# Kernel tuning notes

Hardware: AMD Instinct MI355X
Metric: run time of the kernel (lower is better)

Reference implementation:

```python
import jax, jax.numpy as jnp
import numpy as np
from jax import lax

B, T, PRED, F, L, H = 128, 512, 24, 16, 8, 1024


def _gru_cell(x, h, Wih, Whh, bih, bhh):
    # PyTorch GRU gate math. gi/gh: [B, 3H] in (r, z, n) order.
    gi = x @ Wih.T + bih
    gh = h @ Whh.T + bhh
    i_r, i_z, i_n = jnp.split(gi, 3, axis=-1)
    h_r, h_z, h_n = jnp.split(gh, 3, axis=-1)
    r = jax.nn.sigmoid(i_r + h_r)
    z = jax.nn.sigmoid(i_z + h_z)
    n = jnp.tanh(i_n + r * h_n)
    return (1.0 - z) * n + z * h


def _run_layer(x_seq, Wih, Whh, bih, bhh):
    # x_seq: [B, T, D] -> (outputs [B, T, H], h_T [B, H]); zero initial state as in torch default.
    h0 = jnp.zeros((x_seq.shape[0], Whh.shape[1]), x_seq.dtype)

    def step(h, x_t):
        h = _gru_cell(x_t, h, Wih, Whh, bih, bhh)
        return h, h

    hT, hs = lax.scan(step, h0, jnp.swapaxes(x_seq, 0, 1))
    return jnp.swapaxes(hs, 0, 1), hT


def setup_inputs() -> dict:
    key = jax.random.key(0)
    ks = jax.random.split(key, 20)
    s_in = 1.0 / np.sqrt(H)  # torch default uniform bound ~ 1/sqrt(H); use scaled normal
    d = {
        'feats': jax.random.normal(ks[0], (B, T + PRED - 1, F), jnp.float32),
        'labels': jax.random.normal(ks[1], (B, T, L), jnp.float32),
        'y': jax.random.normal(ks[2], (B, PRED - 1, L), jnp.float32),
        'teacher': 0,
        'enc_Wih0': jax.random.normal(ks[3], (3 * H, F + L), jnp.float32) * s_in,
        'enc_Whh0': jax.random.normal(ks[4], (3 * H, H), jnp.float32) * s_in,
        'enc_bih0': jax.random.normal(ks[5], (3 * H,), jnp.float32) * s_in,
        'enc_bhh0': jax.random.normal(ks[6], (3 * H,), jnp.float32) * s_in,
        'enc_Wih1': jax.random.normal(ks[7], (3 * H, H), jnp.float32) * s_in,
        'enc_Whh1': jax.random.normal(ks[8], (3 * H, H), jnp.float32) * s_in,
        'enc_bih1': jax.random.normal(ks[9], (3 * H,), jnp.float32) * s_in,
        'enc_bhh1': jax.random.normal(ks[10], (3 * H,), jnp.float32) * s_in,
        'dec_Wih': jax.random.normal(ks[11], (3 * H, F + L), jnp.float32) * s_in,
        'dec_Whh': jax.random.normal(ks[12], (3 * H, H), jnp.float32) * s_in,
        'dec_bih': jax.random.normal(ks[13], (3 * H,), jnp.float32) * s_in,
        'dec_bhh': jax.random.normal(ks[14], (3 * H,), jnp.float32) * s_in,
        'fc_W': jax.random.normal(ks[15], (L, H), jnp.float32) * s_in,
        'fc_b': jax.random.normal(ks[16], (L,), jnp.float32) * s_in,
    }
    return d


def reference(feats, labels, y, teacher,
              enc_Wih0, enc_Whh0, enc_bih0, enc_bhh0,
              enc_Wih1, enc_Whh1, enc_bih1, enc_bhh1,
              dec_Wih, dec_Whh, dec_bih, dec_bhh,
              fc_W, fc_b):
    seq_len = labels.shape[1]
    prior = feats[:, :seq_len]                 # [B, T, F]
    post = feats[:, seq_len:]                  # [B, PRED-1, F]
    x = jnp.concatenate([prior, labels], -1)   # [B, T, F+L]

    # 2-layer batch_first GRU encoder; take last layer's output at final time step.
    out0, _ = _run_layer(x, enc_Wih0, enc_Whh0, enc_bih0, enc_bhh0)
    _, h = _run_layer(out0, enc_Wih1, enc_Whh1, enc_bih1, enc_bhh1)  # h: [B, H]

    ps = h @ fc_W.T + fc_b                     # [B, L]
    post_t = jnp.swapaxes(post, 0, 1)          # [PRED-1, B, F]

    if teacher:
        y_t = jnp.swapaxes(y, 0, 1)            # [PRED-1, B, L]

        def step(h, xs):
            f_t, y_i = xs
            xin = jnp.concatenate([f_t, y_i], -1)
            h = _gru_cell(xin, h, dec_Wih, dec_Whh, dec_bih, dec_bhh)
            return h, h @ fc_W.T + fc_b

        _, outs = lax.scan(step, h, (post_t, y_t))
    else:
        def step(carry, f_t):
            h, p = carry
            xin = jnp.concatenate([f_t, p], -1)
            h = _gru_cell(xin, h, dec_Wih, dec_Whh, dec_bih, dec_bhh)
            p = h @ fc_W.T + fc_b
            return (h, p), p

        _, outs = lax.scan(step, (h, ps), post_t)

    return jnp.concatenate([ps[None], outs], 0)  # [PRED, B, L]
```

## Files before the change

### kernel.cpp

```cpp
#include <hip/hip_runtime.h>
#include <cstdint>
#include <cstddef>


typedef _Float16 f16;
typedef f16 f16x8 __attribute__((ext_vector_type(8)));
typedef float f32x4 __attribute__((ext_vector_type(4)));

#define NB 208
#define NT 512
#define H_ 1024
#define HSLOT 131072
#define GSLOT 393216

__device__ __forceinline__ float sigm(float x) { return 1.0f / (1.0f + __expf(-x)); }

__device__ __forceinline__ void gbar(int* flags, int* rel, int phase) {
  __syncthreads();
  const int tid = threadIdx.x;
  if (blockIdx.x == 0) {
    if (tid == 0) {
      __builtin_amdgcn_fence(__ATOMIC_RELEASE, "agent");
      __hip_atomic_store(&flags[0], phase, __ATOMIC_RELAXED, __HIP_MEMORY_SCOPE_AGENT);
    }
    if (tid < NB) {
      while (__hip_atomic_load(&flags[tid], __ATOMIC_RELAXED, __HIP_MEMORY_SCOPE_AGENT) < phase)
        __builtin_amdgcn_s_sleep(1);
    }
    __syncthreads();
    if (tid == 0) {
      __hip_atomic_store(rel, phase, __ATOMIC_RELAXED, __HIP_MEMORY_SCOPE_AGENT);
      __builtin_amdgcn_fence(__ATOMIC_ACQUIRE, "agent");
    }
  } else {
    if (tid == 0) {
      __builtin_amdgcn_fence(__ATOMIC_RELEASE, "agent");
      __hip_atomic_store(&flags[blockIdx.x], phase, __ATOMIC_RELAXED, __HIP_MEMORY_SCOPE_AGENT);
      while (__hip_atomic_load(rel, __ATOMIC_RELAXED, __HIP_MEMORY_SCOPE_AGENT) < phase)
        __builtin_amdgcn_s_sleep(1);
      __builtin_amdgcn_fence(__ATOMIC_ACQUIRE, "agent");
    }
  }
  __syncthreads();
}

__device__ __forceinline__ void fastbar(int* flags2, int* done, int fph, int nl,
                                        bool lead) {
  __syncthreads();
  const int tid = threadIdx.x;
  if (tid == 0)
    __hip_atomic_store(&flags2[blockIdx.x], fph, __ATOMIC_RELAXED, __HIP_MEMORY_SCOPE_AGENT);
  if (lead) {
    if (tid < NB) {
      while (__hip_atomic_load(&flags2[tid], __ATOMIC_RELAXED, __HIP_MEMORY_SCOPE_AGENT) < fph)
        __builtin_amdgcn_s_sleep(1);
    }
    __syncthreads();
    if (tid == 0) {
      __builtin_amdgcn_fence(__ATOMIC_RELEASE, "agent");
      if ((fph & 3) == 0)
        __builtin_amdgcn_fence(__ATOMIC_ACQUIRE, "agent");
      __hip_atomic_fetch_add(done, 1, __ATOMIC_RELAXED, __HIP_MEMORY_SCOPE_AGENT);
    }
  }
  if (tid == 0) {
    const int tgt = fph * nl;
    while (__hip_atomic_load(done, __ATOMIC_RELAXED, __HIP_MEMORY_SCOPE_AGENT) < tgt)
      __builtin_amdgcn_s_sleep(1);
  }
  __syncthreads();
}

__device__ __forceinline__ void stage_W48(const float* __restrict__ W, int Ubase,
                                          f16* Wsh, int tid) {
  for (int i = tid; i < 6144; i += NT) {
    int row = i >> 7;
    int k8 = i & 127;
    const float* src = W + ((size_t)((row >> 4) << 10) + Ubase + (row & 15)) * H_ + (k8 << 3);
    float4 a = *(const float4*)(src);
    float4 b = *(const float4*)(src + 4);
    f16x8 v;
    v[0] = (f16)a.x; v[1] = (f16)a.y; v[2] = (f16)a.z; v[3] = (f16)a.w;
    v[4] = (f16)b.x; v[5] = (f16)b.y; v[6] = (f16)b.z; v[7] = (f16)b.w;
    *(f16x8*)(Wsh + ((row << 10) + ((k8 ^ (row & 7)) << 3))) = v;
  }
}

__device__ __forceinline__ void stage_wih(const float* __restrict__ W, int Ubase,
                                          f16* wih_s, int tid) {
  for (int i = tid; i < 48 * 32; i += NT) {
    int row = i >> 5, k = i & 31;
    float v = (k < 24) ? W[((size_t)((row >> 4) << 10) + Ubase + (row & 15)) * 24 + k] : 0.f;
    wih_s[row * 32 + k] = (f16)v;
  }
}

__device__ __forceinline__ void gemmK1024(const f16* __restrict__ Ahp,
                                          const f16* Wsh, int lane, int wv, int rot,
                                          f32x4& aR, f32x4& aZ, f32x4& aN) {
  const int q = lane >> 4, r = lane & 15;
  const f16* pa = Ahp + (size_t)(wv * 16 + r) * H_ + q * 8;
  const f16* w0 = Wsh + ((0 * 16 + r) << 10);
  const f16* w1 = Wsh + ((1 * 16 + r) << 10);
  const f16* w2 = Wsh + ((2 * 16 + r) << 10);
  const int sw = r & 7;
  f16x8 bh[4][4];
#pragma unroll
  for (int g = 0; g < 3; ++g) {
#pragma unroll
    for (int j = 0; j < 4; ++j) {
      int kk = (g * 4 + j + rot) & 31;
      bh[g][j] = *(const f16x8*)(pa + kk * 32);
    }
  }
#pragma unroll
  for (int g = 0; g < 8; ++g) {
    if (g < 5) {
      int gg = g + 3;
#pragma unroll
      for (int j = 0; j < 4; ++j) {
        int kk = (gg * 4 + j + rot) & 31;
        bh[gg & 3][j] = *(const f16x8*)(pa + kk * 32);
      }
    }
#pragma unroll
    for (int j = 0; j < 4; ++j) {
      int kk = (g * 4 + j + rot) & 31;
      int ko = ((kk * 4 + q) ^ sw) << 3;
      f16x8 B0 = *(const f16x8*)(w0 + ko);
      f16x8 B1 = *(const f16x8*)(w1 + ko);
      f16x8 B2 = *(const f16x8*)(w2 + ko);
      f16x8 Ah = bh[g & 3][j];
      aR = __builtin_amdgcn_mfma_f32_16x16x32_f16(Ah, B0, aR, 0, 0, 0);
      aZ = __builtin_amdgcn_mfma_f32_16x16x32_f16(Ah, B1, aZ, 0, 0, 0);
      aN = __builtin_amdgcn_mfma_f32_16x16x32_f16(Ah, B2, aN, 0, 0, 0);
    }
  }
}

__device__ __forceinline__ void gemmX(const f16* xs, const f16* wih_s, int lane, int wv,
                                      f32x4& aR, f32x4& aZ, f32x4& aNx) {
  const int q = lane >> 4, r = lane & 15;
  f16x8 Ax = *(const f16x8*)(xs + (wv * 16 + r) * 32 + q * 8);
  f16x8 B0 = *(const f16x8*)(wih_s + (0 * 16 + r) * 32 + q * 8);
  f16x8 B1 = *(const f16x8*)(wih_s + (1 * 16 + r) * 32 + q * 8);
  f16x8 B2 = *(const f16x8*)(wih_s + (2 * 16 + r) * 32 + q * 8);
  aR = __builtin_amdgcn_mfma_f32_16x16x32_f16(Ax, B0, aR, 0, 0, 0);
  aZ = __builtin_amdgcn_mfma_f32_16x16x32_f16(Ax, B1, aZ, 0, 0, 0);
  aNx = __builtin_amdgcn_mfma_f32_16x16x32_f16(Ax, B2, aNx, 0, 0, 0);
}

__device__ __forceinline__ void gru_epilogue(const f32x4& aR, const f32x4& aZ,
                                             const f32x4& aNh, const f32x4& aNx,
                                             float bR, float bZ, float bIN, float bHN,
                                             const f16* hph, f16* hoh, int u, int b0) {
#pragma unroll
  for (int i = 0; i < 4; ++i) {
    float rg = sigm(aR[i] + bR);
    float zg = sigm(aZ[i] + bZ);
    float ng = tanhf(aNx[i] + bIN + rg * (aNh[i] + bHN));
    size_t off = (size_t)(b0 + i) * H_ + u;
    float hp = (float)hph[off];
    float hn = (1.f - zg) * ng + zg * hp;
    hoh[off] = (f16)hn;
  }
}

__device__ __forceinline__ void fc_step(const f16* hh, const float* fcW_s,
                                        float fcbv, int fcblk,
                                        int tid, float* out_slice, float* pdst) {
  int b_loc = tid >> 6;
  int l = (tid >> 3) & 7;
  int strip = tid & 7;
  int b = fcblk * 8 + b_loc;
  const f16* ph = hh + (size_t)b * H_ + strip * 128;
  const float* pw = fcW_s + l * H_ + strip * 128;
  float s = 0.f;
  for (int j = 0; j < 128; j += 8) {
    f16x8 a = *(const f16x8*)(ph + j);
#pragma unroll
    for (int e = 0; e < 8; ++e) s += (float)a[e] * pw[j + e];
  }
  s += __shfl_xor(s, 1);
  s += __shfl_xor(s, 2);
  s += __shfl_xor(s, 4);
  if (strip == 0) {
    float v = s + fcbv;
    out_slice[b * 8 + l] = v;
    pdst[b * 8 + l] = v;
  }
}

__global__ __launch_bounds__(NT, 2) void gru_persist(
    const float* __restrict__ feats, const float* __restrict__ labels,
    const float* __restrict__ wih0, const float* __restrict__ whh0,
    const float* __restrict__ bih0, const float* __restrict__ bhh0,
    const float* __restrict__ wih1, const float* __restrict__ whh1,
    const float* __restrict__ bih1, const float* __restrict__ bhh1,
    const float* __restrict__ dwih, const float* __restrict__ dwhh,
    const float* __restrict__ dbih, const float* __restrict__ dbhh,
    const float* __restrict__ fcW, const float* __restrict__ fcb,
    float* __restrict__ out, char* ws) {
  int* flags = (int*)ws;
  int* flags2 = (int*)(ws + 2048);
  int* ctrl = (int*)(ws + 4096);
  f16* h0r = (f16*)(ws + 8192);
  f16* h1r = (f16*)(ws + 8192 + 2097152);
  float* gir = (float*)(ws + 8192 + 4194304);
  float* pbr = (float*)(ws + 8192 + 4194304 + 12582912);

  const int bid = blockIdx.x, tid = threadIdx.x;
  const int lane = tid & 63, wv = tid >> 6;
  const int q = lane >> 4, r = lane & 15;
  const int role = bid >> 6;
  const int Ubase = (bid & 63) << 4;
  const int u = Ubase + r;
  const int b0 = wv * 16 + q * 4;
  const int rot = ((bid >> 3) & 7) << 2;

  __shared__ __align__(16) unsigned char smem[109568];
  __shared__ int s_lead, s_nl;
  f16* Wsh = (f16*)smem;
  f16* xs = (f16*)(smem + 98304);
  f16* wih_s = (f16*)(smem + 106496);
  float* fcW_s = (float*)smem;

  if (bid == 0 && tid >= 1 && tid <= 10) ctrl[tid] = 0;

  {
    uint32_t* z0 = (uint32_t*)(h0r + 7 * HSLOT);
    uint32_t* z1 = (uint32_t*)(h1r + 7 * HSLOT);
    for (int i = bid * NT + tid; i < 65536; i += NB * NT) { z0[i] = 0; z1[i] = 0; }
  }
  for (int i = tid; i < 2048; i += NT) ((uint32_t*)xs)[i] = 0;

  if (role == 0) { stage_W48(whh0, Ubase, Wsh, tid); stage_wih(wih0, Ubase, wih_s, tid); }
  else if (role == 1) stage_W48(wih1, Ubase, Wsh, tid);
  else if (role == 2) stage_W48(whh1, Ubase, Wsh, tid);
  else for (int i = tid; i < 8192; i += NT) fcW_s[i] = fcW[i];

  float bR = 0.f, bZ = 0.f, bIN = 0.f, bHN = 0.f;
  if (role == 0) {
    bR = bih0[u] + bhh0[u]; bZ = bih0[1024 + u] + bhh0[1024 + u];
    bIN = bih0[2048 + u];   bHN = bhh0[2048 + u];
  } else if (role == 2) {
    bR = bih1[u] + bhh1[u]; bZ = bih1[1024 + u] + bhh1[1024 + u];
    bIN = bih1[2048 + u];   bHN = bhh1[2048 + u];
  }
  float fcbv = (role == 3) ? fcb[(tid >> 3) & 7] : 0.f;

  gbar(flags, &ctrl[0], 1);

  if (tid == 0) {
    int xcd;
    asm volatile("s_getreg_b32 %0, hwreg(HW_REG_XCC_ID)" : "=s"(xcd));
    int old = __hip_atomic_fetch_add(&ctrl[2 + (xcd & 7)], 1, __ATOMIC_RELAXED,
                                     __HIP_MEMORY_SCOPE_AGENT);
    int ld = (old == 0) ? 1 : 0;
    if (ld) __hip_atomic_fetch_add(&ctrl[10], 1, __ATOMIC_RELAXED, __HIP_MEMORY_SCOPE_AGENT);
    s_lead = ld;
  }
  gbar(flags, &ctrl[0], 2);
  if (tid == 0) s_nl = __hip_atomic_load(&ctrl[10], __ATOMIC_RELAXED, __HIP_MEMORY_SCOPE_AGENT);
  __syncthreads();
  const bool lead = (s_lead != 0);
  const int NL = s_nl;
  int fp = 0;

  for (int s = 0; s < 514; ++s) {
    if (role == 0 && s < 512) {
      const int row = tid >> 2, k8 = tid & 3;
      float4 xa = {0, 0, 0, 0}, xb = {0, 0, 0, 0};
      if (k8 < 2) {
        const float* fpt = feats + ((size_t)row * 535 + s) * 16 + k8 * 8;
        xa = *(const float4*)fpt; xb = *(const float4*)(fpt + 4);
      } else if (k8 == 2) {
        const float* lp = labels + ((size_t)row * 512 + s) * 8;
        xa = *(const float4*)lp; xb = *(const float4*)(lp + 4);
      }
      const f16* hph = h0r + (size_t)((s + 7) & 7) * HSLOT;
      f16* hoh = h0r + (size_t)(s & 7) * HSLOT;
      f32x4 aR = {0,0,0,0}, aZ = {0,0,0,0}, aN = {0,0,0,0}, aNx = {0,0,0,0};
      gemmK1024(hph, Wsh, lane, wv, rot, aR, aZ, aN);
      if (k8 < 3) {
        f16x8 v;
        v[0] = (f16)xa.x; v[1] = (f16)xa.y; v[2] = (f16)xa.z; v[3] = (f16)xa.w;
        v[4] = (f16)xb.x; v[5] = (f16)xb.y; v[6] = (f16)xb.z; v[7] = (f16)xb.w;
        *(f16x8*)(xs + row * 32 + ((k8 == 2) ? 16 : k8 * 8)) = v;
      }
      __syncthreads();
      gemmX(xs, wih_s, lane, wv, aR, aZ, aNx);
      gru_epilogue(aR, aZ, aN, aNx, bR, bZ, bIN, bHN, hph, hoh, u, b0);
    } else if (role == 1 && s >= 1 && s <= 512) {
      const f16* hph = h0r + (size_t)((s + 7) & 7) * HSLOT;
      f32x4 aR = {0,0,0,0}, aZ = {0,0,0,0}, aN = {0,0,0,0};
      gemmK1024(hph, Wsh, lane, wv, rot, aR, aZ, aN);
      float* dst = gir + (size_t)((s + 7) & 7) * GSLOT;
      *(f32x4*)(dst + (size_t)u * 128 + b0) = aR;
      *(f32x4*)(dst + (size_t)(1024 + u) * 128 + b0) = aZ;
      *(f32x4*)(dst + (size_t)(2048 + u) * 128 + b0) = aN;
    } else if (role == 2 && s >= 2) {
      const f16* hph = h1r + (size_t)((s + 5) & 7) * HSLOT;
      f16* hoh = h1r + (size_t)((s + 6) & 7) * HSLOT;
      const float* gp = gir + (size_t)((s + 6) & 7) * GSLOT;
      f32x4 gR = *(const f32x4*)(gp + (size_t)u * 128 + b0);
      f32x4 gZ = *(const f32x4*)(gp + (size_t)(1024 + u) * 128 + b0);
      f32x4 gN = *(const f32x4*)(gp + (size_t)(2048 + u) * 128 + b0);
      f32x4 aR = {0,0,0,0}, aZ = {0,0,0,0}, aN = {0,0,0,0};
      gemmK1024(hph, Wsh, lane, wv, rot, aR, aZ, aN);
      f32x4 tR = aR + gR, tZ = aZ + gZ;
      gru_epilogue(tR, tZ, aN, gN, bR, bZ, bIN, bHN, hph, hoh, u, b0);
    }
    fastbar(flags2, &ctrl[1], ++fp, NL, lead);
  }

  if (role == 3) {
    const f16* hf = h1r + 7 * HSLOT;
    fc_step(hf, fcW_s, fcbv, bid - 192, tid, out, pbr);
  }
  if (role == 0) {
    stage_W48(dwhh, Ubase, Wsh, tid);
    stage_wih(dwih, Ubase, wih_s, tid);
    bR = dbih[u] + dbhh[u]; bZ = dbih[1024 + u] + dbhh[1024 + u];
    bIN = dbih[2048 + u];   bHN = dbhh[2048 + u];
  }
  fastbar(flags2, &ctrl[1], ++fp, NL, lead);

  for (int d = 0; d < 23; ++d) {
    if (role == 0) {
      const int row = tid >> 2, k8 = tid & 3;
      float4 xa = {0, 0, 0, 0}, xb = {0, 0, 0, 0};
      if (k8 < 2) {
        const float* fpt = feats + ((size_t)row * 535 + 512 + d) * 16 + k8 * 8;
        xa = *(const float4*)fpt; xb = *(const float4*)(fpt + 4);
      } else if (k8 == 2) {
        const float* pp = pbr + (size_t)(d & 7) * 1024 + row * 8;
        xa = *(const float4*)pp; xb = *(const float4*)(pp + 4);
      }
      const f16* hph = h1r + (size_t)((d + 7) & 7) * HSLOT;
      f16* hoh = h1r + (size_t)(d & 7) * HSLOT;
      f32x4 aR = {0,0,0,0}, aZ = {0,0,0,0}, aN = {0,0,0,0}, aNx = {0,0,0,0};
      gemmK1024(hph, Wsh, lane, wv, rot, aR, aZ, aN);
      if (k8 < 3) {
        f16x8 v;
        v[0] = (f16)xa.x; v[1] = (f16)xa.y; v[2] = (f16)xa.z; v[3] = (f16)xa.w;
        v[4] = (f16)xb.x; v[5] = (f16)xb.y; v[6] = (f16)xb.z; v[7] = (f16)xb.w;
        *(f16x8*)(xs + row * 32 + ((k8 == 2) ? 16 : k8 * 8)) = v;
      }
      __syncthreads();
      gemmX(xs, wih_s, lane, wv, aR, aZ, aNx);
      gru_epilogue(aR, aZ, aN, aNx, bR, bZ, bIN, bHN, hph, hoh, u, b0);
    }
    fastbar(flags2, &ctrl[1], ++fp, NL, lead);
    if (role == 3) {
      const f16* hd = h1r + (size_t)(d & 7) * HSLOT;
      fc_step(hd, fcW_s, fcbv, bid - 192, tid,
              out + (size_t)(d + 1) * 1024, pbr + (size_t)((d + 1) & 7) * 1024);
    }
    fastbar(flags2, &ctrl[1], ++fp, NL, lead);
  }
}

extern "C" void kernel_launch(void* const* d_in, const int* in_sizes, int n_in,
                              void* d_out, int out_size, void* d_ws, size_t ws_size,
                              hipStream_t stream) {
  (void)in_sizes; (void)n_in; (void)out_size; (void)ws_size;
  gru_persist<<<NB, NT, 0, stream>>>(
      (const float*)d_in[0], (const float*)d_in[1],
      (const float*)d_in[4], (const float*)d_in[5],
      (const float*)d_in[6], (const float*)d_in[7],
      (const float*)d_in[8], (const float*)d_in[9],
      (const float*)d_in[10], (const float*)d_in[11],
      (const float*)d_in[12], (const float*)d_in[13],
      (const float*)d_in[14], (const float*)d_in[15],
      (const float*)d_in[16], (const float*)d_in[17],
      (float*)d_out, (char*)d_ws);
}
```

Baseline: 7.181 ms.

## Split K-dimension of recurrent GEMM across two wave halves with LDS reduction

Doubles the block to 1024 threads so that each of the 8 batch-row waves is paired with a second wave handling the other half of the K=1024 reduction. Partial gate accumulators from the second half are exchanged through a new LDS buffer and summed before the epilogue. This is meant to halve the per-wave serial MFMA chain on the latency-bound recurrent step. In exchange it adds an extra LDS round trip and block sync per step, enlarges shared memory, and halves the register budget per thread.

Result: slower. 7.364 ms (+2.5%).

```diff
diff --git a/kernel.cpp b/kernel.cpp
--- a/kernel.cpp
+++ b/kernel.cpp
@@ -8,7 +8,7 @@
 typedef float f32x4 __attribute__((ext_vector_type(4)));
 
 #define NB 208
-#define NT 512
+#define NT 1024
 #define H_ 1024
 #define HSLOT 131072
 #define GSLOT 393216
@@ -95,37 +95,38 @@
   }
 }
 
-__device__ __forceinline__ void gemmK1024(const f16* __restrict__ Ahp,
-                                          const f16* Wsh, int lane, int wv, int rot,
-                                          f32x4& aR, f32x4& aZ, f32x4& aN) {
+__device__ __forceinline__ void gemmK512(const f16* __restrict__ Ahp,
+                                         const f16* Wsh, int lane, int wv8,
+                                         int half, int rot,
+                                         f32x4& aR, f32x4& aZ, f32x4& aN) {
   const int q = lane >> 4, r = lane & 15;
-  const f16* pa = Ahp + (size_t)(wv * 16 + r) * H_ + q * 8;
-  const f16* w0 = Wsh + ((0 * 16 + r) << 10);
-  const f16* w1 = Wsh + ((1 * 16 + r) << 10);
-  const f16* w2 = Wsh + ((2 * 16 + r) << 10);
+  const f16* pa = Ahp + (size_t)(wv8 * 16 + r) * H_ + half * 512 + q * 8;
+  const f16* w0 = Wsh + ((0 * 16 + r) << 10) + half * 512;
+  const f16* w1 = Wsh + ((1 * 16 + r) << 10) + half * 512;
+  const f16* w2 = Wsh + ((2 * 16 + r) << 10) + half * 512;
   const int sw = r & 7;
   f16x8 bh[4][4];
 #pragma unroll
   for (int g = 0; g < 3; ++g) {
 #pragma unroll
     for (int j = 0; j < 4; ++j) {
-      int kk = (g * 4 + j + rot) & 31;
+      int kk = (g * 4 + j + rot) & 15;
       bh[g][j] = *(const f16x8*)(pa + kk * 32);
     }
   }
 #pragma unroll
-  for (int g = 0; g < 8; ++g) {
-    if (g < 5) {
+  for (int g = 0; g < 4; ++g) {
+    if (g < 1) {
       int gg = g + 3;
 #pragma unroll
       for (int j = 0; j < 4; ++j) {
-        int kk = (gg * 4 + j + rot) & 31;
+        int kk = (gg * 4 + j + rot) & 15;
         bh[gg & 3][j] = *(const f16x8*)(pa + kk * 32);
       }
     }
 #pragma unroll
     for (int j = 0; j < 4; ++j) {
-      int kk = (g * 4 + j + rot) & 31;
+      int kk = (g * 4 + j + rot) & 15;
       int ko = ((kk * 4 + q) ^ sw) << 3;
       f16x8 B0 = *(const f16x8*)(w0 + ko);
       f16x8 B1 = *(const f16x8*)(w1 + ko);
@@ -138,10 +139,10 @@
   }
 }
 
-__device__ __forceinline__ void gemmX(const f16* xs, const f16* wih_s, int lane, int wv,
+__device__ __forceinline__ void gemmX(const f16* xs, const f16* wih_s, int lane, int wv8,
                                       f32x4& aR, f32x4& aZ, f32x4& aNx) {
   const int q = lane >> 4, r = lane & 15;
-  f16x8 Ax = *(const f16x8*)(xs + (wv * 16 + r) * 32 + q * 8);
+  f16x8 Ax = *(const f16x8*)(xs + (wv8 * 16 + r) * 32 + q * 8);
   f16x8 B0 = *(const f16x8*)(wih_s + (0 * 16 + r) * 32 + q * 8);
   f16x8 B1 = *(const f16x8*)(wih_s + (1 * 16 + r) * 32 + q * 8);
   f16x8 B2 = *(const f16x8*)(wih_s + (2 * 16 + r) * 32 + q * 8);
@@ -169,6 +170,7 @@
 __device__ __forceinline__ void fc_step(const f16* hh, const float* fcW_s,
                                         float fcbv, int fcblk,
                                         int tid, float* out_slice, float* pdst) {
+  if (tid >= 512) return;
   int b_loc = tid >> 6;
   int l = (tid >> 3) & 7;
   int strip = tid & 7;
@@ -191,7 +193,7 @@
   }
 }
 
-__global__ __launch_bounds__(NT, 2) void gru_persist(
+__global__ __launch_bounds__(NT, 4) void gru_persist(
     const float* __restrict__ feats, const float* __restrict__ labels,
     const float* __restrict__ wih0, const float* __restrict__ whh0,
     const float* __restrict__ bih0, const float* __restrict__ bhh0,
@@ -211,18 +213,20 @@
 
   const int bid = blockIdx.x, tid = threadIdx.x;
   const int lane = tid & 63, wv = tid >> 6;
+  const int wv8 = wv & 7, half = wv >> 3;
   const int q = lane >> 4, r = lane & 15;
   const int role = bid >> 6;
   const int Ubase = (bid & 63) << 4;
   const int u = Ubase + r;
-  const int b0 = wv * 16 + q * 4;
-  const int rot = ((bid >> 3) & 7) << 2;
-
-  __shared__ __align__(16) unsigned char smem[109568];
+  const int b0 = wv8 * 16 + q * 4;
+  const int rot = ((bid >> 3) & 3) << 2;
+
+  __shared__ __align__(16) unsigned char smem[134144];
   __shared__ int s_lead, s_nl;
   f16* Wsh = (f16*)smem;
   f16* xs = (f16*)(smem + 98304);
   f16* wih_s = (f16*)(smem + 106496);
+  float* exch = (float*)(smem + 109568);
   float* fcW_s = (float*)smem;
 
   if (bid == 0 && tid >= 1 && tid <= 10) ctrl[tid] = 0;
@@ -271,45 +275,100 @@
     if (role == 0 && s < 512) {
       const int row = tid >> 2, k8 = tid & 3;
       float4 xa = {0, 0, 0, 0}, xb = {0, 0, 0, 0};
-      if (k8 < 2) {
-        const float* fpt = feats + ((size_t)row * 535 + s) * 16 + k8 * 8;
-        xa = *(const float4*)fpt; xb = *(const float4*)(fpt + 4);
-      } else if (k8 == 2) {
-        const float* lp = labels + ((size_t)row * 512 + s) * 8;
-        xa = *(const float4*)lp; xb = *(const float4*)(lp + 4);
+      if (tid < 512) {
+        if (k8 < 2) {
+          const float* fpt = feats + ((size_t)row * 535 + s) * 16 + k8 * 8;
+          xa = *(const float4*)fpt; xb = *(const float4*)(fpt + 4);
+        } else if (k8 == 2) {
+          const float* lp = labels + ((size_t)row * 512 + s) * 8;
+          xa = *(const float4*)lp; xb = *(const float4*)(lp + 4);
+        }
       }
       const f16* hph = h0r + (size_t)((s + 7) & 7) * HSLOT;
       f16* hoh = h0r + (size_t)(s & 7) * HSLOT;
       f32x4 aR = {0,0,0,0}, aZ = {0,0,0,0}, aN = {0,0,0,0}, aNx = {0,0,0,0};
-      gemmK1024(hph, Wsh, lane, wv, rot, aR, aZ, aN);
-      if (k8 < 3) {
+      gemmK512(hph, Wsh, lane, wv8, half, rot, aR, aZ, aN);
+      if (tid < 512 && k8 < 3) {
         f16x8 v;
         v[0] = (f16)xa.x; v[1] = (f16)xa.y; v[2] = (f16)xa.z; v[3] = (f16)xa.w;
         v[4] = (f16)xb.x; v[5] = (f16)xb.y; v[6] = (f16)xb.z; v[7] = (f16)xb.w;
         *(f16x8*)(xs + row * 32 + ((k8 == 2) ? 16 : k8 * 8)) = v;
       }
+      if (half == 1) {
+#pragma unroll
+        for (int i = 0; i < 4; ++i) {
+          exch[0 * 2048 + (b0 + i) * 16 + r] = aR[i];
+          exch[1 * 2048 + (b0 + i) * 16 + r] = aZ[i];
+          exch[2 * 2048 + (b0 + i) * 16 + r] = aN[i];
+        }
+      }
       __syncthreads();
-      gemmX(xs, wih_s, lane, wv, aR, aZ, aNx);
-      gru_epilogue(aR, aZ, aN, aNx, bR, bZ, bIN, bHN, hph, hoh, u, b0);
+      if (half == 0) {
+#pragma unroll
+        for (int i = 0; i < 4; ++i) {
+          aR[i] += exch[0 * 2048 + (b0 + i) * 16 + r];
+          aZ[i] += exch[1 * 2048 + (b0 + i) * 16 + r];
+          aN[i] += exch[2 * 2048 + (b0 + i) * 16 + r];
+        }
+        gemmX(xs, wih_s, lane, wv8, aR, aZ, aNx);
+        gru_epilogue(aR, aZ, aN, aNx, bR, bZ, bIN, bHN, hph, hoh, u, b0);
+      }
     } else if (role == 1 && s >= 1 && s <= 512) {
       const f16* hph = h0r + (size_t)((s + 7) & 7) * HSLOT;
       f32x4 aR = {0,0,0,0}, aZ = {0,0,0,0}, aN = {0,0,0,0};
-      gemmK1024(hph, Wsh, lane, wv, rot, aR, aZ, aN);
-      float* dst = gir + (size_t)((s + 7) & 7) * GSLOT;
-      *(f32x4*)(dst + (size_t)u * 128 + b0) = aR;
-      *(f32x4*)(dst + (size_t)(1024 + u) * 128 + b0) = aZ;
-      *(f32x4*)(dst + (size_t)(2048 + u) * 128 + b0) = aN;
+      gemmK512(hph, Wsh, lane, wv8, half, rot, aR, aZ, aN);
+      if (half == 1) {
+#pragma unroll
+        for (int i = 0; i < 4; ++i) {
+          exch[0 * 2048 + (b0 + i) * 16 + r] = aR[i];
+          exch[1 * 2048 + (b0 + i) * 16 + r] = aZ[i];
+          exch[2 * 2048 + (b0 + i) * 16 + r] = aN[i];
+        }
+      }
+      __syncthreads();
+      if (half == 0) {
+#pragma unroll
+        for (int i = 0; i < 4; ++i) {
+          aR[i] += exch[0 * 2048 + (b0 + i) * 16 + r];
+          aZ[i] += exch[1 * 2048 + (b0 + i) * 16 + r];
+          aN[i] += exch[2 * 2048 + (b0 + i) * 16 + r];
+        }
+        float* dst = gir + (size_t)((s + 7) & 7) * GSLOT;
+        *(f32x4*)(dst + (size_t)u * 128 + b0) = aR;
+        *(f32x4*)(dst + (size_t)(1024 + u) * 128 + b0) = aZ;
+        *(f32x4*)(dst + (size_t)(2048 + u) * 128 + b0) = aN;
+      }
     } else if (role == 2 && s >= 2) {
       const f16* hph = h1r + (size_t)((s + 5) & 7) * HSLOT;
       f16* hoh = h1r + (size_t)((s + 6) & 7) * HSLOT;
       const float* gp = gir + (size_t)((s + 6) & 7) * GSLOT;
-      f32x4 gR = *(const f32x4*)(gp + (size_t)u * 128 + b0);
-      f32x4 gZ = *(const f32x4*)(gp + (size_t)(1024 + u) * 128 + b0);
-      f32x4 gN = *(const f32x4*)(gp + (size_t)(2048 + u) * 128 + b0);
+      f32x4 gR = {0,0,0,0}, gZ = {0,0,0,0}, gN = {0,0,0,0};
+      if (half == 0) {
+        gR = *(const f32x4*)(gp + (size_t)u * 128 + b0);
+        gZ = *(const f32x4*)(gp + (size_t)(1024 + u) * 128 + b0);
+        gN = *(const f32x4*)(gp + (size_t)(2048 + u) * 128 + b0);
+      }
       f32x4 aR = {0,0,0,0}, aZ = {0,0,0,0}, aN = {0,0,0,0};
-      gemmK1024(hph, Wsh, lane, wv, rot, aR, aZ, aN);
-      f32x4 tR = aR + gR, tZ = aZ + gZ;
-      gru_epilogue(tR, tZ, aN, gN, bR, bZ, bIN, bHN, hph, hoh, u, b0);
+      gemmK512(hph, Wsh, lane, wv8, half, rot, aR, aZ, aN);
+      if (half == 1) {
+#pragma unroll
+        for (int i = 0; i < 4; ++i) {
+          exch[0 * 2048 + (b0 + i) * 16 + r] = aR[i];
+          exch[1 * 2048 + (b0 + i) * 16 + r] = aZ[i];
+          exch[2 * 2048 + (b0 + i) * 16 + r] = aN[i];
+        }
+      }
+      __syncthreads();
+      if (half == 0) {
+#pragma unroll
+        for (int i = 0; i < 4; ++i) {
+          aR[i] += exch[0 * 2048 + (b0 + i) * 16 + r];
+          aZ[i] += exch[1 * 2048 + (b0 + i) * 16 + r];
+          aN[i] += exch[2 * 2048 + (b0 + i) * 16 + r];
+        }
+        f32x4 tR = aR + gR, tZ = aZ + gZ;
+        gru_epilogue(tR, tZ, aN, gN, bR, bZ, bIN, bHN, hph, hoh, u, b0);
+      }
     }
     fastbar(flags2, &ctrl[1], ++fp, NL, lead);
   }
@@ -330,26 +389,44 @@
     if (role == 0) {
       const int row = tid >> 2, k8 = tid & 3;
       float4 xa = {0, 0, 0, 0}, xb = {0, 0, 0, 0};
-      if (k8 < 2) {
-        const float* fpt = feats + ((size_t)row * 535 + 512 + d) * 16 + k8 * 8;
-        xa = *(const float4*)fpt; xb = *(const float4*)(fpt + 4);
-      } else if (k8 == 2) {
-        const float* pp = pbr + (size_t)(d & 7) * 1024 + row * 8;
-        xa = *(const float4*)pp; xb = *(const float4*)(pp + 4);
+      if (tid < 512) {
+        if (k8 < 2) {
+          const float* fpt = feats + ((size_t)row * 535 + 512 + d) * 16 + k8 * 8;
+          xa = *(const float4*)fpt; xb = *(const float4*)(fpt + 4);
+        } else if (k8 == 2) {
+          const float* pp = pbr + (size_t)(d & 7) * 1024 + row * 8;
+          xa = *(const float4*)pp; xb = *(const float4*)(pp + 4);
+        }
       }
       const f16* hph = h1r + (size_t)((d + 7) & 7) * HSLOT;
       f16* hoh = h1r + (size_t)(d & 7) * HSLOT;
       f32x4 aR = {0,0,0,0}, aZ = {0,0,0,0}, aN = {0,0,0,0}, aNx = {0,0,0,0};
-      gemmK1024(hph, Wsh, lane, wv, rot, aR, aZ, aN);
-      if (k8 < 3) {
+      gemmK512(hph, Wsh, lane, wv8, half, rot, aR, aZ, aN);
+      if (tid < 512 && k8 < 3) {
         f16x8 v;
         v[0] = (f16)xa.x; v[1] = (f16)xa.y; v[2] = (f16)xa.z; v[3] = (f16)xa.w;
         v[4] = (f16)xb.x; v[5] = (f16)xb.y; v[6] = (f16)xb.z; v[7] = (f16)xb.w;
         *(f16x8*)(xs + row * 32 + ((k8 == 2) ? 16 : k8 * 8)) = v;
       }
+      if (half == 1) {
+#pragma unroll
+        for (int i = 0; i < 4; ++i) {
+          exch[0 * 2048 + (b0 + i) * 16 + r] = aR[i];
+          exch[1 * 2048 + (b0 + i) * 16 + r] = aZ[i];
+          exch[2 * 2048 + (b0 + i) * 16 + r] = aN[i];
+        }
+      }
       __syncthreads();
-      gemmX(xs, wih_s, lane, wv, aR, aZ, aNx);
-      gru_epilogue(aR, aZ, aN, aNx, bR, bZ, bIN, bHN, hph, hoh, u, b0);
+      if (half == 0) {
+#pragma unroll
+        for (int i = 0; i < 4; ++i) {
+          aR[i] += exch[0 * 2048 + (b0 + i) * 16 + r];
+          aZ[i] += exch[1 * 2048 + (b0 + i) * 16 + r];
+          aN[i] += exch[2 * 2048 + (b0 + i) * 16 + r];
+        }
+        gemmX(xs, wih_s, lane, wv8, aR, aZ, aNx);
+        gru_epilogue(aR, aZ, aN, aNx, bR, bZ, bIN, bHN, hph, hoh, u, b0);
+      }
     }
     fastbar(flags2, &ctrl[1], ++fp, NL, lead);
     if (role == 3) {
```

## Make grid barrier hierarchical per XCD with local leader release flags

Applied to the files above, without the earlier changes.

Rebuilds the per-step grid barrier as a two-level tree. Each XCD's leader block polls only the arrival flags of blocks on its own die, then joins a global counter with the other leaders and publishes a per-XCD release flag. Non-leader blocks spin only on their XCD's release word instead of all blocks polling one global counter. The aim is to cut cross-die atomic contention and barrier latency across the ~540 barriers; the risk is that ranks and counts from the setup fetch-add must stay consistent.

After: 6.435 ms. 1.12x faster.

```diff
diff --git a/kernel.cpp b/kernel.cpp
--- a/kernel.cpp
+++ b/kernel.cpp
@@ -44,31 +44,37 @@
   __syncthreads();
 }
 
-__device__ __forceinline__ void fastbar(int* flags2, int* done, int fph, int nl,
-                                        bool lead) {
+__device__ __forceinline__ void fastbar(int* xaf, int* xrel, int* gdone,
+                                        int fph, int nl, int xcd, int rank,
+                                        int cnt, bool lead) {
   __syncthreads();
   const int tid = threadIdx.x;
   if (tid == 0)
-    __hip_atomic_store(&flags2[blockIdx.x], fph, __ATOMIC_RELAXED, __HIP_MEMORY_SCOPE_AGENT);
+    __hip_atomic_store(&xaf[(xcd << 6) + rank], fph, __ATOMIC_RELAXED, __HIP_MEMORY_SCOPE_AGENT);
   if (lead) {
-    if (tid < NB) {
-      while (__hip_atomic_load(&flags2[tid], __ATOMIC_RELAXED, __HIP_MEMORY_SCOPE_AGENT) < fph)
+    if (tid < cnt) {
+      while (__hip_atomic_load(&xaf[(xcd << 6) + tid], __ATOMIC_RELAXED, __HIP_MEMORY_SCOPE_AGENT) < fph)
         __builtin_amdgcn_s_sleep(1);
     }
     __syncthreads();
     if (tid == 0) {
       __builtin_amdgcn_fence(__ATOMIC_RELEASE, "agent");
+      __hip_atomic_fetch_add(gdone, 1, __ATOMIC_RELAXED, __HIP_MEMORY_SCOPE_AGENT);
+      const int tgt = fph * nl;
+      while (__hip_atomic_load(gdone, __ATOMIC_RELAXED, __HIP_MEMORY_SCOPE_AGENT) < tgt)
+        __builtin_amdgcn_s_sleep(1);
       if ((fph & 3) == 0)
         __builtin_amdgcn_fence(__ATOMIC_ACQUIRE, "agent");
-      __hip_atomic_fetch_add(done, 1, __ATOMIC_RELAXED, __HIP_MEMORY_SCOPE_AGENT);
-    }
-  }
-  if (tid == 0) {
-    const int tgt = fph * nl;
-    while (__hip_atomic_load(done, __ATOMIC_RELAXED, __HIP_MEMORY_SCOPE_AGENT) < tgt)
-      __builtin_amdgcn_s_sleep(1);
-  }
-  __syncthreads();
+      __hip_atomic_store(&xrel[xcd << 4], fph, __ATOMIC_RELAXED, __HIP_MEMORY_SCOPE_AGENT);
+    }
+    __syncthreads();
+  } else {
+    if (tid == 0) {
+      while (__hip_atomic_load(&xrel[xcd << 4], __ATOMIC_RELAXED, __HIP_MEMORY_SCOPE_AGENT) < fph)
+        __builtin_amdgcn_s_sleep(1);
+    }
+    __syncthreads();
+  }
 }
 
 __device__ __forceinline__ void stage_W48(const float* __restrict__ W, int Ubase,
@@ -202,8 +208,9 @@
     const float* __restrict__ fcW, const float* __restrict__ fcb,
     float* __restrict__ out, char* ws) {
   int* flags = (int*)ws;
-  int* flags2 = (int*)(ws + 2048);
+  int* xaf = (int*)(ws + 2048);
   int* ctrl = (int*)(ws + 4096);
+  int* xrel = ctrl + 64;
   f16* h0r = (f16*)(ws + 8192);
   f16* h1r = (f16*)(ws + 8192 + 2097152);
   float* gir = (float*)(ws + 8192 + 4194304);
@@ -219,7 +226,7 @@
   const int rot = ((bid >> 3) & 7) << 2;
 
   __shared__ __align__(16) unsigned char smem[109568];
-  __shared__ int s_lead, s_nl;
+  __shared__ int s_lead, s_nl, s_xcd, s_rank, s_cnt;
   f16* Wsh = (f16*)smem;
   f16* xs = (f16*)(smem + 98304);
   f16* wih_s = (f16*)(smem + 106496);
@@ -254,17 +261,21 @@
   if (tid == 0) {
     int xcd;
     asm volatile("s_getreg_b32 %0, hwreg(HW_REG_XCC_ID)" : "=s"(xcd));
-    int old = __hip_atomic_fetch_add(&ctrl[2 + (xcd & 7)], 1, __ATOMIC_RELAXED,
+    xcd &= 7;
+    int old = __hip_atomic_fetch_add(&ctrl[2 + xcd], 1, __ATOMIC_RELAXED,
                                      __HIP_MEMORY_SCOPE_AGENT);
     int ld = (old == 0) ? 1 : 0;
     if (ld) __hip_atomic_fetch_add(&ctrl[10], 1, __ATOMIC_RELAXED, __HIP_MEMORY_SCOPE_AGENT);
-    s_lead = ld;
+    s_lead = ld; s_xcd = xcd; s_rank = old;
   }
   gbar(flags, &ctrl[0], 2);
-  if (tid == 0) s_nl = __hip_atomic_load(&ctrl[10], __ATOMIC_RELAXED, __HIP_MEMORY_SCOPE_AGENT);
+  if (tid == 0) {
+    s_nl = __hip_atomic_load(&ctrl[10], __ATOMIC_RELAXED, __HIP_MEMORY_SCOPE_AGENT);
+    s_cnt = __hip_atomic_load(&ctrl[2 + s_xcd], __ATOMIC_RELAXED, __HIP_MEMORY_SCOPE_AGENT);
+  }
   __syncthreads();
   const bool lead = (s_lead != 0);
-  const int NL = s_nl;
+  const int NL = s_nl, XCD = s_xcd, RANK = s_rank, CNT = s_cnt;
   int fp = 0;
 
   for (int s = 0; s < 514; ++s) {
@@ -311,7 +322,7 @@
       f32x4 tR = aR + gR, tZ = aZ + gZ;
       gru_epilogue(tR, tZ, aN, gN, bR, bZ, bIN, bHN, hph, hoh, u, b0);
     }
-    fastbar(flags2, &ctrl[1], ++fp, NL, lead);
+    fastbar(xaf, xrel, &ctrl[1], ++fp, NL, XCD, RANK, CNT, lead);
   }
 
   if (role == 3) {
@@ -324,7 +335,7 @@
     bR = dbih[u] + dbhh[u]; bZ = dbih[1024 + u] + dbhh[1024 + u];
     bIN = dbih[2048 + u];   bHN = dbhh[2048 + u];
   }
-  fastbar(flags2, &ctrl[1], ++fp, NL, lead);
+  fastbar(xaf, xrel, &ctrl[1], ++fp, NL, XCD, RANK, CNT, lead);
 
   for (int d = 0; d < 23; ++d) {
     if (role == 0) {
@@ -351,13 +362,13 @@
       gemmX(xs, wih_s, lane, wv, aR, aZ, aNx);
       gru_epilogue(aR, aZ, aN, aNx, bR, bZ, bIN, bHN, hph, hoh, u, b0);
     }
-    fastbar(flags2, &ctrl[1], ++fp, NL, lead);
+    fastbar(xaf, xrel, &ctrl[1], ++fp, NL, XCD, RANK, CNT, lead);
     if (role == 3) {
       const f16* hd = h1r + (size_t)(d & 7) * HSLOT;
       fc_step(hd, fcW_s, fcbv, bid - 192, tid,
               out + (size_t)(d + 1) * 1024, pbr + (size_t)((d + 1) & 7) * 1024);
     }
-    fastbar(flags2, &ctrl[1], ++fp, NL, lead);
+    fastbar(xaf, xrel, &ctrl[1], ++fp, NL, XCD, RANK, CNT, lead);
   }
 }
 
```
